# Performance work log

Hardware: AMD Instinct MI355X
Metric: run time of the kernel (lower is better)

## Reference

```python
import jax, jax.numpy as jnp
import numpy as np


def _normal_distance(n1, n2):
    # Cosine-style normal distance: 1 - <n1, n2>. The original module stubs
    # this as 0; we use the canonical mesh-normal loss so the cdist+argmin+
    # gather chain is exercised end-to-end.
    return 1.0 - jnp.sum(n1 * n2, axis=-1)


def setup_inputs() -> dict:
    key = jax.random.key(0)
    k1, k2, k3, k4 = jax.random.split(key, 4)
    N, M = 8192, 32768
    pred_pts = jax.random.normal(k1, (1, N, 3), dtype=jnp.float32)
    pred_nrm = jax.random.normal(k2, (1, N, 3), dtype=jnp.float32)
    gt_pts = jax.random.normal(k3, (1, M, 3), dtype=jnp.float32)
    gt_nrm = jax.random.normal(k4, (1, M, 3), dtype=jnp.float32)
    # unit normals, as on a real mesh
    pred_nrm = pred_nrm / jnp.linalg.norm(pred_nrm, axis=-1, keepdims=True)
    gt_nrm = gt_nrm / jnp.linalg.norm(gt_nrm, axis=-1, keepdims=True)
    return {
        "predicted_points_batch": pred_pts,
        "predicted_normals_batch": pred_nrm,
        "gt_points_batch": gt_pts,
        "gt_normals_batch": gt_nrm,
    }


def reference(predicted_points_batch, predicted_normals_batch,
              gt_points_batch, gt_normals_batch):
    # Original forward returns inside the first loop iteration -> element 0 only.
    p = predicted_points_batch[0]    # [N,3]
    pn = predicted_normals_batch[0]  # [N,3]
    g = gt_points_batch[0]           # [M,3]
    gn = gt_normals_batch[0]         # [M,3]

    # Squared pairwise distances (monotone in true cdist; only argmin is used).
    # d2[i,j] = |p_i|^2 + |g_j|^2 - 2 p_i . g_j   -> one [N,M] intermediate.
    d2 = (jnp.sum(p * p, axis=1)[:, None]
          + jnp.sum(g * g, axis=1)[None, :]
          - 2.0 * (p @ g.T))                      # [N,M]

    gt_idx = jnp.argmin(d2, axis=1)    # nearest gt point per predicted point, [N]
    pr_idx = jnp.argmin(d2, axis=0)    # nearest predicted point per gt point, [M]

    nearest_gt_normals = gn[gt_idx]    # [N,3]
    nearest_pr_normals = pn[pr_idx]    # [M,3]

    dist1 = _normal_distance(pn, nearest_gt_normals)  # [N]
    dist2 = _normal_distance(gn, nearest_pr_normals)  # [M]
    return jnp.mean(dist1) + jnp.mean(dist2)
```

## Files before the change

### kernel.cpp

```cpp
#include <hip/hip_runtime.h>
#include <stdint.h>
#include <float.h>

#define BLK 256
#define IPT 8
#define OWNERS (BLK * IPT)
#define SLICE2 256
#define SLICE1 128
#define SUB 64

typedef unsigned long long ull;

__device__ __forceinline__ unsigned int ford(float f) {
    int b = __float_as_int(f);
    return (b >= 0) ? ((unsigned)b ^ 0x80000000u) : ~(unsigned)b;
}
__device__ __forceinline__ float ford_inv(unsigned int u) {
    int b = (u & 0x80000000u) ? (int)(u ^ 0x80000000u) : (int)~u;
    return __int_as_float(b);
}

__global__ __launch_bounds__(BLK) void nn_slices(
    const float* __restrict__ p, const float* __restrict__ g,
    ull* __restrict__ wsR, ull* __restrict__ wsC,
    float* __restrict__ out, int N, int M)
{
    __shared__ float4 sb[SLICE2];

    if (blockIdx.x == 0 && threadIdx.x == 0) *out = 0.0f;

    const int rowBlocks = (N / OWNERS) * (M / SLICE2);
    const float* A; const float* B; ull* ws; int id, nSlices, NO;
    if ((int)blockIdx.x < rowBlocks) {
        id = blockIdx.x;             A = p; B = g; ws = wsR; nSlices = M / SLICE2; NO = N;
    } else {
        id = blockIdx.x - rowBlocks; A = g; B = p; ws = wsC; nSlices = N / SLICE2; NO = M;
    }
    const int chunk = id / nSlices;
    const int j = id - chunk * nSlices;
    const int s0 = j * SLICE2;

    {
        int s = s0 + threadIdx.x;
        float bx = B[3 * s], by = B[3 * s + 1], bz = B[3 * s + 2];
        float w = fmaf(bz, bz, fmaf(by, by, bx * bx));
        sb[threadIdx.x] = make_float4(bx, by, bz, w);
    }

    const int o0 = chunk * OWNERS + threadIdx.x;
    float ax[IPT], ay[IPT], az[IPT], best[IPT];
    int base[IPT];
#pragma unroll
    for (int r = 0; r < IPT; ++r) {
        int o = o0 + r * BLK;
        ax[r] = -2.0f * A[3 * o];
        ay[r] = -2.0f * A[3 * o + 1];
        az[r] = -2.0f * A[3 * o + 2];
        best[r] = FLT_MAX;
        base[r] = s0;
    }
    __syncthreads();

    for (int st = 0; st < SLICE2; st += SUB) {
        float prev[IPT];
#pragma unroll
        for (int r = 0; r < IPT; ++r) prev[r] = best[r];
#pragma unroll 2
        for (int k = st; k < st + SUB; k += 2) {
            float4 q0 = sb[k];
            float4 q1 = sb[k + 1];
#pragma unroll
            for (int r = 0; r < IPT; ++r) {
                float v0 = fmaf(ax[r], q0.x, fmaf(ay[r], q0.y, fmaf(az[r], q0.z, q0.w)));
                float v1 = fmaf(ax[r], q1.x, fmaf(ay[r], q1.y, fmaf(az[r], q1.z, q1.w)));
                best[r] = fminf(fminf(v0, v1), best[r]);
            }
        }
#pragma unroll
        for (int r = 0; r < IPT; ++r)
            if (best[r] < prev[r]) base[r] = s0 + st;
    }

    ull* dst = ws + (size_t)j * NO;
#pragma unroll
    for (int r = 0; r < IPT; ++r)
        dst[o0 + r * BLK] = ((ull)ford(best[r]) << 32) | (unsigned)base[r];
}

__global__ __launch_bounds__(BLK) void reduce_fin(
    const ull* __restrict__ wsR, const ull* __restrict__ wsC,
    const float* __restrict__ p, const float* __restrict__ g,
    const float* __restrict__ pn, const float* __restrict__ gn,
    float* __restrict__ out, int N, int M, float invN, float invM)
{
    int t = blockIdx.x * BLK + threadIdx.x;
    float c = 0.0f;
    if (t < N + M) {
        const float* A; const float* B; const float* An; const float* Bn;
        const ull* ws; int o, K, NO; float inv;
        if (t < N) { o = t;     A = p; B = g; An = pn; Bn = gn; ws = wsR; K = M / SLICE2; NO = N; inv = invN; }
        else       { o = t - N; A = g; B = p; An = gn; Bn = pn; ws = wsC; K = N / SLICE2; NO = M; inv = invM; }

        ull bestp = ws[o];
#pragma unroll 4
        for (int jj = 1; jj < K; ++jj) {
            ull v2 = ws[(size_t)jj * NO + o];
            bestp = (v2 < bestp) ? v2 : bestp;
        }

        float ax = -2.0f * A[3 * o];
        float ay = -2.0f * A[3 * o + 1];
        float az = -2.0f * A[3 * o + 2];
        float bestf = ford_inv((unsigned int)(bestp >> 32));
        int b0 = (int)(bestp & 0xffffffffull);

        int idx = 0x7fffffff;
#pragma unroll 4
        for (int jj = 0; jj < SUB; ++jj) {
            int s = b0 + jj;
            float bx = B[3 * s], by = B[3 * s + 1], bz = B[3 * s + 2];
            float w = fmaf(bz, bz, fmaf(by, by, bx * bx));
            float v = fmaf(ax, bx, fmaf(ay, by, fmaf(az, bz, w)));
            int cand = (v == bestf) ? s : 0x7fffffff;
            idx = (cand < idx) ? cand : idx;
        }
        if (idx == 0x7fffffff) idx = b0;

        float d = An[3 * o] * Bn[3 * idx] + An[3 * o + 1] * Bn[3 * idx + 1]
                + An[3 * o + 2] * Bn[3 * idx + 2];
        c = (1.0f - d) * inv;
    }
#pragma unroll
    for (int off = 32; off > 0; off >>= 1) c += __shfl_down(c, off, 64);
    __shared__ float partial[BLK / 64];
    if ((threadIdx.x & 63) == 0) partial[threadIdx.x >> 6] = c;
    __syncthreads();
    if (threadIdx.x == 0) {
        float s = 0.0f;
#pragma unroll
        for (int w = 0; w < BLK / 64; ++w) s += partial[w];
        atomicAdd(out, s);
    }
}

__global__ __launch_bounds__(BLK) void nn_min_dual(
    const float* __restrict__ p, const float* __restrict__ g,
    ull* __restrict__ rowmin, ull* __restrict__ colmin,
    int rowBlocks, int rowSlices, int colSlices)
{
    __shared__ float4 sb[SLICE1];
    const float* A; const float* B; ull* outmin; int id, nSlices;
    if ((int)blockIdx.x < rowBlocks) {
        id = blockIdx.x;             A = p; B = g; outmin = rowmin; nSlices = rowSlices;
    } else {
        id = blockIdx.x - rowBlocks; A = g; B = p; outmin = colmin; nSlices = colSlices;
    }
    const int chunk = id / nSlices;
    const int slice = id - chunk * nSlices;
    const int s0 = slice * SLICE1;
    if (threadIdx.x < SLICE1) {
        int s = s0 + threadIdx.x;
        float bx = B[3 * s], by = B[3 * s + 1], bz = B[3 * s + 2];
        float w = fmaf(bz, bz, fmaf(by, by, bx * bx));
        sb[threadIdx.x] = make_float4(bx, by, bz, w);
    }
    const int o0 = chunk * OWNERS + threadIdx.x;
    float ax[IPT], ay[IPT], az[IPT], best[IPT];
    int base[IPT];
#pragma unroll
    for (int r = 0; r < IPT; ++r) {
        int o = o0 + r * BLK;
        ax[r] = -2.0f * A[3 * o]; ay[r] = -2.0f * A[3 * o + 1]; az[r] = -2.0f * A[3 * o + 2];
        best[r] = FLT_MAX; base[r] = s0;
    }
    __syncthreads();
    for (int st = 0; st < SLICE1; st += SUB) {
        float prev[IPT];
#pragma unroll
        for (int r = 0; r < IPT; ++r) prev[r] = best[r];
#pragma unroll 2
        for (int k = st; k < st + SUB; k += 2) {
            float4 q0 = sb[k]; float4 q1 = sb[k + 1];
#pragma unroll
            for (int r = 0; r < IPT; ++r) {
                float v0 = fmaf(ax[r], q0.x, fmaf(ay[r], q0.y, fmaf(az[r], q0.z, q0.w)));
                float v1 = fmaf(ax[r], q1.x, fmaf(ay[r], q1.y, fmaf(az[r], q1.z, q1.w)));
                best[r] = fminf(fminf(v0, v1), best[r]);
            }
        }
#pragma unroll
        for (int r = 0; r < IPT; ++r)
            if (best[r] < prev[r]) base[r] = s0 + st;
    }
#pragma unroll
    for (int r = 0; r < IPT; ++r) {
        ull packed = ((ull)ford(best[r]) << 32) | (unsigned)base[r];
        atomicMin(&outmin[o0 + r * BLK], packed);
    }
}

__global__ __launch_bounds__(BLK) void finalize_legacy(
    const ull* __restrict__ rowmin, const ull* __restrict__ colmin,
    const float* __restrict__ p, const float* __restrict__ g,
    const float* __restrict__ pn, const float* __restrict__ gn,
    float* __restrict__ out, int N, int M, float invN, float invM)
{
    int t = blockIdx.x * BLK + threadIdx.x;
    float c = 0.0f;
    if (t < N + M) {
        const float* A; const float* B; const float* An; const float* Bn;
        ull packed; int o; float inv;
        if (t < N) { o = t;     A = p; B = g; An = pn; Bn = gn; packed = rowmin[o]; inv = invN; }
        else       { o = t - N; A = g; B = p; An = gn; Bn = pn; packed = colmin[o]; inv = invM; }
        float ax = -2.0f * A[3 * o], ay = -2.0f * A[3 * o + 1], az = -2.0f * A[3 * o + 2];
        float bestf = ford_inv((unsigned int)(packed >> 32));
        int b0 = (int)(packed & 0xffffffffull);
        int idx = 0x7fffffff;
#pragma unroll 4
        for (int jj = 0; jj < SUB; ++jj) {
            int s = b0 + jj;
            float bx = B[3 * s], by = B[3 * s + 1], bz = B[3 * s + 2];
            float w = fmaf(bz, bz, fmaf(by, by, bx * bx));
            float v = fmaf(ax, bx, fmaf(ay, by, fmaf(az, bz, w)));
            int cand = (v == bestf) ? s : 0x7fffffff;
            idx = (cand < idx) ? cand : idx;
        }
        if (idx == 0x7fffffff) idx = b0;
        float d = An[3 * o] * Bn[3 * idx] + An[3 * o + 1] * Bn[3 * idx + 1]
                + An[3 * o + 2] * Bn[3 * idx + 2];
        c = (1.0f - d) * inv;
    }
#pragma unroll
    for (int off = 32; off > 0; off >>= 1) c += __shfl_down(c, off, 64);
    __shared__ float partial[BLK / 64];
    if ((threadIdx.x & 63) == 0) partial[threadIdx.x >> 6] = c;
    __syncthreads();
    if (threadIdx.x == 0) {
        float s = 0.0f;
#pragma unroll
        for (int w = 0; w < BLK / 64; ++w) s += partial[w];
        atomicAdd(out, s);
    }
}

extern "C" void kernel_launch(void* const* d_in, const int* in_sizes, int n_in,
                              void* d_out, int out_size, void* d_ws, size_t ws_size,
                              hipStream_t stream) {
    const float* p  = (const float*)d_in[0];
    const float* pn = (const float*)d_in[1];
    const float* g  = (const float*)d_in[2];
    const float* gn = (const float*)d_in[3];
    const int N = in_sizes[0] / 3;
    const int M = in_sizes[2] / 3;
    float* out = (float*)d_out;

    const size_t needR = (size_t)(M / SLICE2) * N * sizeof(ull);
    const size_t needC = (size_t)(N / SLICE2) * M * sizeof(ull);
    const bool geomOK = (N % OWNERS) == 0 && (M % OWNERS) == 0 &&
                        (N % SLICE2) == 0 && (M % SLICE2) == 0 &&
                        ((N + M) % BLK) == 0;

    if (geomOK && ws_size >= needR + needC) {
        ull* wsR = (ull*)d_ws;
        ull* wsC = wsR + (size_t)(M / SLICE2) * N;
        const int blocks = (N / OWNERS) * (M / SLICE2) + (M / OWNERS) * (N / SLICE2);
        nn_slices<<<blocks, BLK, 0, stream>>>(p, g, wsR, wsC, out, N, M);
        reduce_fin<<<(N + M) / BLK, BLK, 0, stream>>>(
            wsR, wsC, p, g, pn, gn, out, N, M, 1.0f / N, 1.0f / M);
    } else {
        ull* rowmin = (ull*)d_ws;
        ull* colmin = rowmin + N;
        hipMemsetAsync(d_ws, 0xFF, (size_t)(N + M) * sizeof(ull), stream);
        hipMemsetAsync(d_out, 0, sizeof(float), stream);
        const int rowSlices = M / SLICE1;
        const int colSlices = N / SLICE1;
        const int rowBlocks = (N / OWNERS) * rowSlices;
        const int colBlocks = (M / OWNERS) * colSlices;
        nn_min_dual<<<rowBlocks + colBlocks, BLK, 0, stream>>>(
            p, g, rowmin, colmin, rowBlocks, rowSlices, colSlices);
        int tot = N + M;
        finalize_legacy<<<(tot + BLK - 1) / BLK, BLK, 0, stream>>>(
            rowmin, colmin, p, g, pn, gn, out, N, M, 1.0f / N, 1.0f / M);
    }
}
```

Measured before the change: 122.4 us.

## Fuse slice min and finalize into one kernel using atomicMin and last-block reduction

Replaces the two-kernel design, which wrote per-slice partial minima to a large workspace and reduced them in a second kernel, with one fused kernel. Each block folds its packed (distance, base) pair into a per-point slot with 64-bit atomicMin. The last block per owner chunk, found with a counter, resolves the exact index and the normal distance, and the last chunk writes the final sum. Slice size drops from 256 to 128, doubling the block count. This removes the workspace write/read traffic and one launch, but adds a memset, many global atomics and a serialized tail on the last-arriving blocks.

```diff
diff --git a/kernel.cpp b/kernel.cpp
--- a/kernel.cpp
+++ b/kernel.cpp
@@ -5,11 +5,11 @@
 #define BLK 256
 #define IPT 8
 #define OWNERS (BLK * IPT)
-#define SLICE2 256
-#define SLICE1 128
+#define SLICE 128
 #define SUB 64
 
 typedef unsigned long long ull;
+typedef unsigned int u32;
 
 __device__ __forceinline__ unsigned int ford(float f) {
     int b = __float_as_int(f);
@@ -20,27 +20,38 @@
     return __int_as_float(b);
 }
 
-__global__ __launch_bounds__(BLK) void nn_slices(
+__global__ __launch_bounds__(BLK) void nn_fused(
     const float* __restrict__ p, const float* __restrict__ g,
-    ull* __restrict__ wsR, ull* __restrict__ wsC,
-    float* __restrict__ out, int N, int M)
+    const float* __restrict__ pn, const float* __restrict__ gn,
+    ull* __restrict__ mins, u32* __restrict__ ctr, u32* __restrict__ done,
+    float* __restrict__ csum, float* __restrict__ out, int N, int M)
 {
-    __shared__ float4 sb[SLICE2];
-
-    if (blockIdx.x == 0 && threadIdx.x == 0) *out = 0.0f;
-
-    const int rowBlocks = (N / OWNERS) * (M / SLICE2);
-    const float* A; const float* B; ull* ws; int id, nSlices, NO;
-    if ((int)blockIdx.x < rowBlocks) {
-        id = blockIdx.x;             A = p; B = g; ws = wsR; nSlices = M / SLICE2; NO = N;
+    __shared__ float4 sb[SLICE];
+    __shared__ u32 lastFlag;
+    __shared__ float partial[BLK / 64];
+
+    const int rowSlices = M / SLICE;
+    const int colSlices = N / SLICE;
+    const int rowChunks = N / OWNERS;
+    const int rowBlocks = rowChunks * rowSlices;
+    const int nChunks = rowChunks + (M / OWNERS);
+
+    const float* A; const float* B; const float* An; const float* Bn;
+    ull* minsSide; int id, nSlices; float inv;
+    const bool rowSide = (int)blockIdx.x < rowBlocks;
+    if (rowSide) {
+        id = blockIdx.x;             A = p; B = g; An = pn; Bn = gn;
+        minsSide = mins;     nSlices = rowSlices; inv = 1.0f / (float)N;
     } else {
-        id = blockIdx.x - rowBlocks; A = g; B = p; ws = wsC; nSlices = N / SLICE2; NO = M;
+        id = blockIdx.x - rowBlocks; A = g; B = p; An = gn; Bn = pn;
+        minsSide = mins + N; nSlices = colSlices; inv = 1.0f / (float)M;
     }
     const int chunk = id / nSlices;
-    const int j = id - chunk * nSlices;
-    const int s0 = j * SLICE2;
-
-    {
+    const int slice = id - chunk * nSlices;
+    const int chunkG = rowSide ? chunk : (rowChunks + chunk);
+    const int s0 = slice * SLICE;
+
+    if (threadIdx.x < SLICE) {
         int s = s0 + threadIdx.x;
         float bx = B[3 * s], by = B[3 * s + 1], bz = B[3 * s + 2];
         float w = fmaf(bz, bz, fmaf(by, by, bx * bx));
@@ -61,7 +72,7 @@
     }
     __syncthreads();
 
-    for (int st = 0; st < SLICE2; st += SUB) {
+    for (int st = 0; st < SLICE; st += SUB) {
         float prev[IPT];
 #pragma unroll
         for (int r = 0; r < IPT; ++r) prev[r] = best[r];
@@ -81,38 +92,33 @@
             if (best[r] < prev[r]) base[r] = s0 + st;
     }
 
-    ull* dst = ws + (size_t)j * NO;
-#pragma unroll
-    for (int r = 0; r < IPT; ++r)
-        dst[o0 + r * BLK] = ((ull)ford(best[r]) << 32) | (unsigned)base[r];
-}
-
-__global__ __launch_bounds__(BLK) void reduce_fin(
-    const ull* __restrict__ wsR, const ull* __restrict__ wsC,
-    const float* __restrict__ p, const float* __restrict__ g,
-    const float* __restrict__ pn, const float* __restrict__ gn,
-    float* __restrict__ out, int N, int M, float invN, float invM)
-{
-    int t = blockIdx.x * BLK + threadIdx.x;
+#pragma unroll
+    for (int r = 0; r < IPT; ++r) {
+        ull packed = ((ull)ford(best[r]) << 32) | (unsigned)base[r];
+        atomicMin(&minsSide[o0 + r * BLK], packed);
+    }
+
+    __syncthreads();
+    if (threadIdx.x == 0) {
+        __threadfence();
+        u32 old = atomicAdd(&ctr[chunkG], 1u);
+        lastFlag = (old == (u32)(nSlices - 2)) ? 1u : 0u;
+    }
+    __syncthreads();
+    if (!lastFlag) return;
+    __threadfence();
+
     float c = 0.0f;
-    if (t < N + M) {
-        const float* A; const float* B; const float* An; const float* Bn;
-        const ull* ws; int o, K, NO; float inv;
-        if (t < N) { o = t;     A = p; B = g; An = pn; Bn = gn; ws = wsR; K = M / SLICE2; NO = N; inv = invN; }
-        else       { o = t - N; A = g; B = p; An = gn; Bn = pn; ws = wsC; K = N / SLICE2; NO = M; inv = invM; }
-
-        ull bestp = ws[o];
-#pragma unroll 4
-        for (int jj = 1; jj < K; ++jj) {
-            ull v2 = ws[(size_t)jj * NO + o];
-            bestp = (v2 < bestp) ? v2 : bestp;
-        }
-
-        float ax = -2.0f * A[3 * o];
-        float ay = -2.0f * A[3 * o + 1];
-        float az = -2.0f * A[3 * o + 2];
-        float bestf = ford_inv((unsigned int)(bestp >> 32));
-        int b0 = (int)(bestp & 0xffffffffull);
+#pragma unroll
+    for (int r = 0; r < IPT; ++r) {
+        int o = chunk * OWNERS + threadIdx.x + r * BLK;
+        ull packed = __hip_atomic_load(&minsSide[o], __ATOMIC_RELAXED,
+                                       __HIP_MEMORY_SCOPE_AGENT);
+        float axx = -2.0f * A[3 * o];
+        float ayy = -2.0f * A[3 * o + 1];
+        float azz = -2.0f * A[3 * o + 2];
+        float bestf = ford_inv((unsigned int)(packed >> 32));
+        int b0 = (int)(packed & 0xffffffffull);
 
         int idx = 0x7fffffff;
 #pragma unroll 4
@@ -120,7 +126,7 @@
             int s = b0 + jj;
             float bx = B[3 * s], by = B[3 * s + 1], bz = B[3 * s + 2];
             float w = fmaf(bz, bz, fmaf(by, by, bx * bx));
-            float v = fmaf(ax, bx, fmaf(ay, by, fmaf(az, bz, w)));
+            float v = fmaf(axx, bx, fmaf(ayy, by, fmaf(azz, bz, w)));
             int cand = (v == bestf) ? s : 0x7fffffff;
             idx = (cand < idx) ? cand : idx;
         }
@@ -128,18 +134,28 @@
 
         float d = An[3 * o] * Bn[3 * idx] + An[3 * o + 1] * Bn[3 * idx + 1]
                 + An[3 * o + 2] * Bn[3 * idx + 2];
-        c = (1.0f - d) * inv;
-    }
+        c += (1.0f - d) * inv;
+    }
+
 #pragma unroll
     for (int off = 32; off > 0; off >>= 1) c += __shfl_down(c, off, 64);
-    __shared__ float partial[BLK / 64];
     if ((threadIdx.x & 63) == 0) partial[threadIdx.x >> 6] = c;
     __syncthreads();
     if (threadIdx.x == 0) {
         float s = 0.0f;
 #pragma unroll
         for (int w = 0; w < BLK / 64; ++w) s += partial[w];
-        atomicAdd(out, s);
+        __hip_atomic_store(&csum[chunkG], s, __ATOMIC_RELAXED, __HIP_MEMORY_SCOPE_AGENT);
+        __threadfence();
+        u32 od = atomicAdd(done, 1u);
+        if (od == (u32)(nChunks - 2)) {
+            __threadfence();
+            float tot = 0.0f;
+            for (int k2 = 0; k2 < nChunks; ++k2)
+                tot += __hip_atomic_load(&csum[k2], __ATOMIC_RELAXED,
+                                         __HIP_MEMORY_SCOPE_AGENT);
+            *out = tot;
+        }
     }
 }
 
@@ -148,7 +164,7 @@
     ull* __restrict__ rowmin, ull* __restrict__ colmin,
     int rowBlocks, int rowSlices, int colSlices)
 {
-    __shared__ float4 sb[SLICE1];
+    __shared__ float4 sb[SLICE];
     const float* A; const float* B; ull* outmin; int id, nSlices;
     if ((int)blockIdx.x < rowBlocks) {
         id = blockIdx.x;             A = p; B = g; outmin = rowmin; nSlices = rowSlices;
@@ -157,8 +173,8 @@
     }
     const int chunk = id / nSlices;
     const int slice = id - chunk * nSlices;
-    const int s0 = slice * SLICE1;
-    if (threadIdx.x < SLICE1) {
+    const int s0 = slice * SLICE;
+    if (threadIdx.x < SLICE) {
         int s = s0 + threadIdx.x;
         float bx = B[3 * s], by = B[3 * s + 1], bz = B[3 * s + 2];
         float w = fmaf(bz, bz, fmaf(by, by, bx * bx));
@@ -174,7 +190,7 @@
         best[r] = FLT_MAX; base[r] = s0;
     }
     __syncthreads();
-    for (int st = 0; st < SLICE1; st += SUB) {
+    for (int st = 0; st < SLICE; st += SUB) {
         float prev[IPT];
 #pragma unroll
         for (int r = 0; r < IPT; ++r) prev[r] = best[r];
@@ -254,28 +270,36 @@
     const int M = in_sizes[2] / 3;
     float* out = (float*)d_out;
 
-    const size_t needR = (size_t)(M / SLICE2) * N * sizeof(ull);
-    const size_t needC = (size_t)(N / SLICE2) * M * sizeof(ull);
+    const int rowSlices = M / SLICE;
+    const int colSlices = N / SLICE;
+    const int rowChunks = N / OWNERS;
+    const int colChunks = M / OWNERS;
+    const int nChunks = rowChunks + colChunks;
+
+    const size_t minsBytes = (size_t)(N + M) * sizeof(ull);
+    const size_t initBytes = minsBytes + (size_t)(nChunks + 1) * sizeof(u32);
+    const size_t needBytes = initBytes + (size_t)nChunks * sizeof(float);
+
     const bool geomOK = (N % OWNERS) == 0 && (M % OWNERS) == 0 &&
-                        (N % SLICE2) == 0 && (M % SLICE2) == 0 &&
-                        ((N + M) % BLK) == 0;
-
-    if (geomOK && ws_size >= needR + needC) {
-        ull* wsR = (ull*)d_ws;
-        ull* wsC = wsR + (size_t)(M / SLICE2) * N;
-        const int blocks = (N / OWNERS) * (M / SLICE2) + (M / OWNERS) * (N / SLICE2);
-        nn_slices<<<blocks, BLK, 0, stream>>>(p, g, wsR, wsC, out, N, M);
-        reduce_fin<<<(N + M) / BLK, BLK, 0, stream>>>(
-            wsR, wsC, p, g, pn, gn, out, N, M, 1.0f / N, 1.0f / M);
+                        (N % SLICE) == 0 && (M % SLICE) == 0 &&
+                        rowSlices >= 2 && colSlices >= 2 && nChunks >= 2;
+
+    if (geomOK && ws_size >= needBytes) {
+        ull* mins = (ull*)d_ws;
+        u32* ctr  = (u32*)((char*)d_ws + minsBytes);
+        u32* done = ctr + nChunks;
+        float* csum = (float*)(done + 1);
+        hipMemsetAsync(d_ws, 0xFF, initBytes, stream);
+        const int blocks = rowChunks * rowSlices + colChunks * colSlices;
+        nn_fused<<<blocks, BLK, 0, stream>>>(
+            p, g, pn, gn, mins, ctr, done, csum, out, N, M);
     } else {
         ull* rowmin = (ull*)d_ws;
         ull* colmin = rowmin + N;
         hipMemsetAsync(d_ws, 0xFF, (size_t)(N + M) * sizeof(ull), stream);
         hipMemsetAsync(d_out, 0, sizeof(float), stream);
-        const int rowSlices = M / SLICE1;
-        const int colSlices = N / SLICE1;
-        const int rowBlocks = (N / OWNERS) * rowSlices;
-        const int colBlocks = (M / OWNERS) * colSlices;
+        const int rowBlocks = rowChunks * rowSlices;
+        const int colBlocks = colChunks * colSlices;
         nn_min_dual<<<rowBlocks + colBlocks, BLK, 0, stream>>>(
             p, g, rowmin, colmin, rowBlocks, rowSlices, colSlices);
         int tot = N + M;
```

Result: slower. 346.3 us (+182.9%).
